# Kernel tuning notes

Hardware: AMD Instinct MI355X
Metric: run time of the kernel (lower is better)

## Reference

```python
import jax, jax.numpy as jnp
import numpy as np

DIVISOR = 2.0
NEGATIVE_SLOPE = 0.01


def setup_inputs() -> dict:
    key = jax.random.key(0)
    k1, k2, k3 = jax.random.split(key, 3)
    x = jax.random.normal(k1, (32, 128, 130, 130), dtype=jnp.float32)
    weight = jax.random.normal(k2, (256, 128, 3, 3), dtype=jnp.float32) * 0.05
    bias = jax.random.normal(k3, (256,), dtype=jnp.float32)
    return {"x": x, "weight": weight, "bias": bias}


def reference(x, weight, bias):
    # conv2d, stride=1, padding=0 (VALID), NCHW / OIHW layout
    y = jax.lax.conv_general_dilated(
        x, weight,
        window_strides=(1, 1),
        padding='VALID',
        dimension_numbers=('NCHW', 'OIHW', 'NCHW'),
    )
    y = y + bias[None, :, None, None]
    y = y * (1.0 / DIVISOR)
    # fused LeakyReLU epilogue
    return jnp.where(y >= 0, y, y * NEGATIVE_SLOPE)
```

## Files before the change

kernel.cpp:

```cpp
#include <hip/hip_runtime.h>
#include <hip/hip_bf16.h>
#include <stdint.h>

typedef __bf16 bf16x8 __attribute__((ext_vector_type(8)));
typedef float  f32x4  __attribute__((ext_vector_type(4)));

#define NSLOPE 0.01f

#define NB   32
#define CIN  128
#define HIN  130
#define WIN  130
#define KOUT 256
#define POUT 128
#define QOUT 128
#define HWIN (HIN*WIN)
#define PQ   (POUT*QOUT)

#define XP_BYTES 138444800ull
#define WP_ELEMS (2*3*3*KOUT*64)

#define WS_BYTES  16384
#define XT_OFF    32768
#define LDS_TOTAL (32768 + 16640)

#define SB0()  __builtin_amdgcn_sched_barrier(0)
#define VMW(n) asm volatile("s_waitcnt vmcnt(" #n ")" ::: "memory")

__device__ __forceinline__ unsigned short f2bf(float f) {
    unsigned u = __builtin_bit_cast(unsigned, f);
    u += 0x7FFFu + ((u >> 16) & 1u);
    return (unsigned short)(u >> 16);
}

__device__ __forceinline__ void g2lds16(const void* g, void* l) {
    __builtin_amdgcn_global_load_lds(
        (const __attribute__((address_space(1))) void*)g,
        (__attribute__((address_space(3))) void*)l,
        16, 0, 0);
}

__global__ __launch_bounds__(256) void k_conv_xw(const float* __restrict__ X,
                                                 const float* __restrict__ W,
                                                 unsigned short* __restrict__ Xp,
                                                 unsigned short* __restrict__ Wp) {
    __shared__ unsigned int tile[64*131];
    const int tid = threadIdx.x;

    if (blockIdx.x >= NB*HIN) {
        int e = (blockIdx.x - NB*HIN)*256 + tid;
        if (e < WP_ELEMS) {
            int ci = e & 63;
            int k  = (e >> 6) & 255;
            int rsIdx = e >> 14;
            int cc = rsIdx / 9; int rem = rsIdx - cc*9; int r = rem / 3, s = rem - r*3;
            int c = cc*64 + ci;
            Wp[e] = f2bf(W[(size_t)k*1152 + (size_t)c*9 + r*3 + s]);
        }
        return;
    }

    const int b = blockIdx.x;
    const int n = b / 130, h = b - n*130;
    const size_t in0 = (size_t)n*(CIN*(size_t)HWIN) + (size_t)h*WIN;
    for (int fi = tid; fi < 64*130; fi += 256) {
        const int c2 = fi / 130, w = fi - c2*130;
        const float lo = X[in0 + (size_t)(2*c2  )*HWIN + w];
        const float hi = X[in0 + (size_t)(2*c2+1)*HWIN + w];
        tile[c2*131 + w] = (unsigned)f2bf(lo) | ((unsigned)f2bf(hi) << 16);
    }
    __syncthreads();
    unsigned int* outp = (unsigned int*)(Xp + (size_t)b*(WIN*CIN));
    for (int oi = tid; oi < 2080; oi += 256) {
        const int w = oi >> 4, j4 = (oi & 15) << 2;
        uint4 v;
        v.x = tile[(j4+0)*131 + w];
        v.y = tile[(j4+1)*131 + w];
        v.z = tile[(j4+2)*131 + w];
        v.w = tile[(j4+3)*131 + w];
        *(uint4*)(outp + w*64 + j4) = v;
    }
}

__device__ __forceinline__ void stage_w128(const unsigned short* __restrict__ Wp,
                                           unsigned char* lds, int rsidx, int kh, int tid) {
    const unsigned short* wbase = Wp + (size_t)rsidx*(KOUT*64) + (size_t)(kh*128)*64;
    #pragma unroll
    for (int it = 0; it < 8; ++it) {
        const int g    = it*128 + tid;
        const int phys = g << 4;
        const int row  = phys >> 7;
        const int cib  = (phys & 127) ^ ((row & 7) << 4);
        g2lds16(wbase + (size_t)row*64 + (cib >> 1), lds + phys);
    }
}

__device__ __forceinline__ void stage_x128(const unsigned short* __restrict__ Xp,
                                           unsigned char* lds, int n, int h, int cc, int tid) {
    const unsigned short* xbase = Xp + ((size_t)((n*HIN + h)*WIN))*CIN + cc*64;
    #pragma unroll
    for (int it = 0; it < 9; ++it) {
        const int g = it*128 + tid;
        if (g < 1040) {
            const int phys = g << 4;
            const int w    = phys >> 7;
            const int cib  = (phys & 127) ^ ((w & 7) << 4);
            g2lds16(xbase + (size_t)w*CIN + (cib >> 1), lds + phys);
        }
    }
}

template<int PRIO>
__device__ __forceinline__ void conv_body(
    const unsigned short* __restrict__ Xp,
    const unsigned short* __restrict__ Wp,
    const float* __restrict__ bias,
    float* __restrict__ out,
    unsigned char* smem, int tid, int L)
{
    const int lane = tid & 63;
    const int wm   = tid >> 6;
    const int l15  = lane & 15;
    const int kg16 = (lane >> 4) << 4;

    const int kh = L & 1;
    const int np = L >> 1;
    const int p  = np & 127;
    const int n  = np >> 7;

    unsigned char* xt = smem + XT_OFF;

    f32x4 acc[4][8];
    #pragma unroll
    for (int i = 0; i < 4; ++i)
        #pragma unroll
        for (int j = 0; j < 8; ++j)
            acc[i][j] = (f32x4){0.f, 0.f, 0.f, 0.f};

    stage_x128(Xp, xt, n, p, 0, tid);
    stage_w128(Wp, smem, 0, kh, tid);

    #pragma unroll 1
    for (int t = 0; t < 18; ++t) {
        const int cc  = t / 9;
        const int rem = t - cc*9;
        const int r   = rem / 3;
        const int s   = rem - r*3;
        unsigned char* wsR = smem + (t & 1)*WS_BYTES;

        if (s == 0 && t > 0)
            stage_x128(Xp, xt, n, p + r, cc, tid);
        if (t < 17) {
            stage_w128(Wp, smem + ((t + 1) & 1)*WS_BYTES, t + 1, kh, tid);
            VMW(8);
        } else {
            VMW(0);
        }
        __builtin_amdgcn_s_barrier();
        SB0();

        #pragma unroll
        for (int kq = 0; kq < 2; ++kq) {
            const int cib0 = kq*64 + kg16;
            bf16x8 A[4], B[8];
            #pragma unroll
            for (int mf = 0; mf < 4; ++mf) {
                const int row = wm*64 + mf*16 + l15;
                A[mf] = *(const bf16x8*)(wsR + row*128 + (cib0 ^ ((row & 7) << 4)));
            }
            #pragma unroll
            for (int nf = 0; nf < 8; ++nf) {
                const int g = nf*16 + l15 + s;
                B[nf] = *(const bf16x8*)(xt + g*128 + (cib0 ^ ((g & 7) << 4)));
            }
            __builtin_amdgcn_s_setprio(PRIO + 1);
            #pragma unroll
            for (int mf = 0; mf < 4; ++mf)
                #pragma unroll
                for (int nf = 0; nf < 8; ++nf)
                    acc[mf][nf] = __builtin_amdgcn_mfma_f32_16x16x32_bf16(
                        A[mf], B[nf], acc[mf][nf], 0, 0, 0);
            __builtin_amdgcn_s_setprio(PRIO);
        }

        SB0();
        __builtin_amdgcn_s_barrier();
    }

    const int kg = lane >> 4;
    #pragma unroll
    for (int mf = 0; mf < 4; ++mf) {
        const int kb = kh*128 + wm*64 + mf*16 + kg*4;
        const float4 bv = *(const float4*)(bias + kb);
        const float bj[4] = {bv.x, bv.y, bv.z, bv.w};
        #pragma unroll
        for (int nf = 0; nf < 8; ++nf) {
            const int q = nf*16 + l15;
            const size_t base = (((size_t)n*KOUT + kb)*POUT + p)*QOUT + q;
            #pragma unroll
            for (int j = 0; j < 4; ++j) {
                float y = (acc[mf][nf][j] + bj[j]) * 0.5f;
                out[base + (size_t)j*PQ] = (y >= 0.f) ? y : y*NSLOPE;
            }
        }
    }
}

__global__ __launch_bounds__(128, 2) void k_conv_main(
    const unsigned short* __restrict__ Xp,
    const unsigned short* __restrict__ Wp,
    const float* __restrict__ bias,
    float* __restrict__ out)
{
    __shared__ __align__(16) unsigned char smem[LDS_TOTAL];

    const int L = ((blockIdx.x & 7) << 10) | (blockIdx.x >> 3);

    if (blockIdx.x & 1) {
        __builtin_amdgcn_s_setprio(1);
        conv_body<1>(Xp, Wp, bias, out, smem, threadIdx.x, L);
    } else {
        conv_body<0>(Xp, Wp, bias, out, smem, threadIdx.x, L);
    }
}

extern "C" void kernel_launch(void* const* d_in, const int* in_sizes, int n_in,
                              void* d_out, int out_size, void* d_ws, size_t ws_size,
                              hipStream_t stream) {
    const float* X = (const float*)d_in[0];
    const float* W = (const float*)d_in[1];
    const float* B = (const float*)d_in[2];
    float* out = (float*)d_out;
    unsigned short* Xp = (unsigned short*)d_ws;
    unsigned short* Wp = (unsigned short*)((char*)d_ws + XP_BYTES);

    k_conv_xw  <<<NB*HIN + (WP_ELEMS + 255)/256, 256, 0, stream>>>(X, W, Xp, Wp);
    k_conv_main<<<8192, 128, 0, stream>>>(Xp, Wp, B, out);
}
```

Measured before the change: 476.7 us.

## Split K-chunks to 32 channels with double-buffered X and W LDS staging

Restructures the conv main loop from 18 steps of 64 input channels into 36 steps of 32 channels. Both the weight tile and the input row tile are now double-buffered, and the next input row is prefetched mid-iteration. The weight layout and the LDS swizzle change to fit the new 32-channel chunks. LDS use drops from about 49KB to about 33KB, which is meant to allow more resident blocks and hide load latency. In exchange there are twice as many barriers and less MFMA work per sync.

Result: faster. 414.2 us (-13.1%).

```diff
diff --git a/kernel.cpp b/kernel.cpp
--- a/kernel.cpp
+++ b/kernel.cpp
@@ -18,11 +18,10 @@
 #define PQ   (POUT*QOUT)
 
 #define XP_BYTES 138444800ull
-#define WP_ELEMS (2*3*3*KOUT*64)
-
-#define WS_BYTES  16384
-#define XT_OFF    32768
-#define LDS_TOTAL (32768 + 16640)
+#define WP_ELEMS (36*256*32)
+
+#define XS_BASE   16384
+#define LDS_TOTAL 33024
 
 #define SB0()  __builtin_amdgcn_sched_barrier(0)
 #define VMW(n) asm volatile("s_waitcnt vmcnt(" #n ")" ::: "memory")
@@ -50,12 +49,15 @@
     if (blockIdx.x >= NB*HIN) {
         int e = (blockIdx.x - NB*HIN)*256 + tid;
         if (e < WP_ELEMS) {
-            int ci = e & 63;
-            int k  = (e >> 6) & 255;
-            int rsIdx = e >> 14;
-            int cc = rsIdx / 9; int rem = rsIdx - cc*9; int r = rem / 3, s = rem - r*3;
-            int c = cc*64 + ci;
-            Wp[e] = f2bf(W[(size_t)k*1152 + (size_t)c*9 + r*3 + s]);
+            int ci5 = e & 31;
+            int k   = (e >> 5) & 255;
+            int srs = e >> 13;
+            int cc = srs / 18;
+            int kq = (srs / 9) & 1;
+            int rr = (srs / 3) % 3;
+            int s  = srs % 3;
+            int c  = cc*64 + kq*32 + ci5;
+            Wp[e] = f2bf(W[(size_t)k*1152 + (size_t)c*9 + rr*3 + s]);
         }
         return;
     }
@@ -82,30 +84,33 @@
     }
 }
 
-__device__ __forceinline__ void stage_w128(const unsigned short* __restrict__ Wp,
-                                           unsigned char* lds, int rsidx, int kh, int tid) {
-    const unsigned short* wbase = Wp + (size_t)rsidx*(KOUT*64) + (size_t)(kh*128)*64;
-    #pragma unroll
-    for (int it = 0; it < 8; ++it) {
+__device__ __forceinline__ void stage_w32(const unsigned short* __restrict__ Wp,
+                                          unsigned char* lds, int srs, int kh, int tid) {
+    const unsigned short* wb = Wp + (size_t)srs*8192 + (size_t)(kh*128)*32;
+    #pragma unroll
+    for (int it = 0; it < 4; ++it) {
         const int g    = it*128 + tid;
-        const int phys = g << 4;
-        const int row  = phys >> 7;
-        const int cib  = (phys & 127) ^ ((row & 7) << 4);
-        g2lds16(wbase + (size_t)row*64 + (cib >> 1), lds + phys);
-    }
-}
-
-__device__ __forceinline__ void stage_x128(const unsigned short* __restrict__ Xp,
-                                           unsigned char* lds, int n, int h, int cc, int tid) {
-    const unsigned short* xbase = Xp + ((size_t)((n*HIN + h)*WIN))*CIN + cc*64;
-    #pragma unroll
-    for (int it = 0; it < 9; ++it) {
+        const int prow = g >> 3;
+        const int off  = (g & 7) << 4;
+        const int kl   = prow*2 + (off >> 6);
+        const int c    = (off & 63) ^ ((prow & 3) << 4);
+        g2lds16(wb + (size_t)kl*32 + (c >> 1), lds + (g << 4));
+    }
+}
+
+__device__ __forceinline__ void stage_x32(const unsigned short* __restrict__ Xp,
+                                          unsigned char* lds, int n, int h,
+                                          int cc, int kq, int tid) {
+    const unsigned short* xb = Xp + ((size_t)(n*HIN + h)*WIN)*CIN + cc*64 + kq*32;
+    #pragma unroll
+    for (int it = 0; it < 5; ++it) {
         const int g = it*128 + tid;
-        if (g < 1040) {
-            const int phys = g << 4;
-            const int w    = phys >> 7;
-            const int cib  = (phys & 127) ^ ((w & 7) << 4);
-            g2lds16(xbase + (size_t)w*CIN + (cib >> 1), lds + phys);
+        if (g < 520) {
+            const int prow = g >> 3;
+            const int off  = (g & 7) << 4;
+            const int w    = prow*2 + (off >> 6);
+            const int c    = (off & 63) ^ ((prow & 3) << 4);
+            g2lds16(xb + (size_t)w*CIN + (c >> 1), lds + (g << 4));
         }
     }
 }
@@ -121,14 +126,16 @@
     const int lane = tid & 63;
     const int wm   = tid >> 6;
     const int l15  = lane & 15;
-    const int kg16 = (lane >> 4) << 4;
+    const int kg   = lane >> 4;
 
     const int kh = L & 1;
     const int np = L >> 1;
     const int p  = np & 127;
     const int n  = np >> 7;
 
-    unsigned char* xt = smem + XT_OFF;
+    const int klh   = wm*64 + l15;
+    const int aBase = (klh >> 1)*128 + ((klh & 1) << 6)
+                    + ((kg*16) ^ (((klh >> 1) & 3) << 4));
 
     f32x4 acc[4][8];
     #pragma unroll
@@ -137,57 +144,65 @@
         for (int j = 0; j < 8; ++j)
             acc[i][j] = (f32x4){0.f, 0.f, 0.f, 0.f};
 
-    stage_x128(Xp, xt, n, p, 0, tid);
-    stage_w128(Wp, smem, 0, kh, tid);
-
+    stage_x32(Xp, smem + XS_BASE, n, p, 0, 0, tid);
+    stage_w32(Wp, smem, 0, kh, tid);
+    VMW(0);
+    __builtin_amdgcn_s_barrier();
+    SB0();
+
+    int u = 0;
     #pragma unroll 1
-    for (int t = 0; t < 18; ++t) {
-        const int cc  = t / 9;
-        const int rem = t - cc*9;
-        const int r   = rem / 3;
-        const int s   = rem - r*3;
-        unsigned char* wsR = smem + (t & 1)*WS_BYTES;
-
-        if (s == 0 && t > 0)
-            stage_x128(Xp, xt, n, p + r, cc, tid);
-        if (t < 17) {
-            stage_w128(Wp, smem + ((t + 1) & 1)*WS_BYTES, t + 1, kh, tid);
-            VMW(8);
-        } else {
-            VMW(0);
-        }
-        __builtin_amdgcn_s_barrier();
-        SB0();
-
-        #pragma unroll
-        for (int kq = 0; kq < 2; ++kq) {
-            const int cib0 = kq*64 + kg16;
-            bf16x8 A[4], B[8];
-            #pragma unroll
-            for (int mf = 0; mf < 4; ++mf) {
-                const int row = wm*64 + mf*16 + l15;
-                A[mf] = *(const bf16x8*)(wsR + row*128 + (cib0 ^ ((row & 7) << 4)));
-            }
-            #pragma unroll
-            for (int nf = 0; nf < 8; ++nf) {
-                const int g = nf*16 + l15 + s;
-                B[nf] = *(const bf16x8*)(xt + g*128 + (cib0 ^ ((g & 7) << 4)));
-            }
-            __builtin_amdgcn_s_setprio(PRIO + 1);
-            #pragma unroll
-            for (int mf = 0; mf < 4; ++mf)
+    for (int cw = 0; cw < 4; ++cw) {
+        #pragma unroll 1
+        for (int r = 0; r < 3; ++r) {
+            const int xi = cw*3 + r;
+            unsigned char* xs = smem + XS_BASE + (xi & 1)*8320;
+            #pragma unroll 1
+            for (int s = 0; s < 3; ++s, ++u) {
+                unsigned char* wsR = smem + (u & 1)*8192;
+
+                if (u < 35) {
+                    stage_w32(Wp, smem + ((u + 1) & 1)*8192, u + 1, kh, tid);
+                    VMW(4);
+                } else {
+                    VMW(0);
+                }
+                if (s == 1 && xi < 11) {
+                    const int ncw = (r == 2) ? cw + 1 : cw;
+                    const int nr  = (r == 2) ? 0 : r + 1;
+                    stage_x32(Xp, smem + XS_BASE + ((xi + 1) & 1)*8320,
+                              n, p + nr, ncw >> 1, ncw & 1, tid);
+                }
+                __builtin_amdgcn_s_barrier();
+                SB0();
+
+                const int wl    = l15 + s;
+                const int bBase = (wl >> 1)*128 + ((wl & 1) << 6)
+                                + ((kg*16) ^ (((wl >> 1) & 3) << 4));
+
+                bf16x8 A[4], B[8];
+                #pragma unroll
+                for (int mf = 0; mf < 4; ++mf)
+                    A[mf] = *(const bf16x8*)(wsR + aBase + mf*1024);
                 #pragma unroll
                 for (int nf = 0; nf < 8; ++nf)
-                    acc[mf][nf] = __builtin_amdgcn_mfma_f32_16x16x32_bf16(
-                        A[mf], B[nf], acc[mf][nf], 0, 0, 0);
-            __builtin_amdgcn_s_setprio(PRIO);
-        }
-
-        SB0();
-        __builtin_amdgcn_s_barrier();
-    }
-
-    const int kg = lane >> 4;
+                    B[nf] = *(const bf16x8*)(xs + bBase + nf*1024);
+
+                __builtin_amdgcn_s_setprio(PRIO + 1);
+                #pragma unroll
+                for (int mf = 0; mf < 4; ++mf)
+                    #pragma unroll
+                    for (int nf = 0; nf < 8; ++nf)
+                        acc[mf][nf] = __builtin_amdgcn_mfma_f32_16x16x32_bf16(
+                            A[mf], B[nf], acc[mf][nf], 0, 0, 0);
+                __builtin_amdgcn_s_setprio(PRIO);
+
+                SB0();
+                __builtin_amdgcn_s_barrier();
+            }
+        }
+    }
+
     #pragma unroll
     for (int mf = 0; mf < 4; ++mf) {
         const int kb = kh*128 + wm*64 + mf*16 + kg*4;
```
